# Kernel optimization log

Hardware: AMD Instinct MI355X
Metric: run time of the kernel (lower is better)

Reference implementation:

```python
import jax, jax.numpy as jnp
import numpy as np

B, N, C, H, W_, K, POS = 1, 100000, 128, 256, 256, 4, 36


def setup_inputs() -> dict:
    key = jax.random.key(0)
    ks = jax.random.split(key, 12)
    inp = {}
    # query coords in [-1, 1] (grid_sample normalized space)
    inp["query"] = jax.random.uniform(ks[0], (B, N, 3), jnp.float32, -1.0, 1.0)
    inp["pe"] = jax.random.normal(ks[1], (B, N, POS), jnp.float32)
    for i, p in enumerate(["xy", "xz", "yz"]):
        inp[f"feat_{p}"] = jax.random.normal(ks[2 + i], (B, C, H, W_), jnp.float32)
        inp[f"Wa_{p}"] = jax.random.normal(ks[5 + i], (POS, K), jnp.float32) * 0.1
        inp[f"ba_{p}"] = jnp.zeros((K,), jnp.float32)
        # offsets initialized to zero in the module; use small random so sampling is non-trivial
        inp[f"Wo_{p}"] = jax.random.normal(ks[8 + i], (POS, 2 * K), jnp.float32) * 0.02
        inp[f"bo_{p}"] = jnp.zeros((2 * K,), jnp.float32)
    return inp


def _bilinear_border(feat, gx, gy):
    """F.grid_sample(feat, grid, align_corners=False, padding_mode='border').
    feat: [B,C,H,W]; gx,gy: [B,N,K] normalized x (width) and y (height) coords.
    Returns [B,C,N,K]."""
    b, c, h, w = feat.shape
    # unnormalize (align_corners=False) then border-clip
    x = jnp.clip(((gx + 1.0) * w - 1.0) * 0.5, 0.0, w - 1.0)
    y = jnp.clip(((gy + 1.0) * h - 1.0) * 0.5, 0.0, h - 1.0)
    x0 = jnp.floor(x)
    y0 = jnp.floor(y)
    wx = x - x0  # [B,N,K]
    wy = y - y0
    xi0 = x0.astype(jnp.int32)
    yi0 = y0.astype(jnp.int32)
    xi1 = jnp.minimum(xi0 + 1, w - 1)
    yi1 = jnp.minimum(yi0 + 1, h - 1)
    ff = feat.reshape(b, c, h * w)
    gather = jax.vmap(lambda f, lin: f[:, lin])  # [C,HW],[N,K] -> [C,N,K]
    v00 = gather(ff, yi0 * w + xi0)
    v01 = gather(ff, yi0 * w + xi1)
    v10 = gather(ff, yi1 * w + xi0)
    v11 = gather(ff, yi1 * w + xi1)
    wx_ = wx[:, None]
    wy_ = wy[:, None]
    return (v00 * (1.0 - wx_) * (1.0 - wy_) + v01 * wx_ * (1.0 - wy_)
            + v10 * (1.0 - wx_) * wy_ + v11 * wx_ * wy_)


def _sample_plane(coords, pe, feat, Wa, ba, Wo, bo):
    b, n, _ = coords.shape
    attn = jax.nn.softmax(pe @ Wa + ba, axis=-1)            # [B,N,K]
    off = (pe @ Wo + bo).reshape(b, n, K, 2)                 # [B,N,K,2]
    sc = coords[:, :, None, :] + off                         # [B,N,K,2]
    # torch code flips last dim before grid_sample: grid x = sc[...,1], y = sc[...,0]
    sampled = _bilinear_border(feat, sc[..., 1], sc[..., 0])  # [B,C,N,K]
    out = jnp.einsum('bcnk,bnk->bnc', sampled, attn)         # weighted sum over K
    return out


def reference(query, pe, feat_xy, feat_xz, feat_yz,
              Wa_xy, ba_xy, Wo_xy, bo_xy,
              Wa_xz, ba_xz, Wo_xz, bo_xz,
              Wa_yz, ba_yz, Wo_yz, bo_yz):
    idx_xy = jnp.array([0, 1])
    idx_xz = jnp.array([0, 2])
    idx_yz = jnp.array([1, 2])
    f_xy = _sample_plane(query[..., idx_xy], pe, feat_xy, Wa_xy, ba_xy, Wo_xy, bo_xy)
    f_xz = _sample_plane(query[..., idx_xz], pe, feat_xz, Wa_xz, ba_xz, Wo_xz, bo_xz)
    f_yz = _sample_plane(query[..., idx_yz], pe, feat_yz, Wa_yz, ba_yz, Wo_yz, bo_yz)
    return f_xy + f_xz + f_yz
```

## Files before the change

kernel.cpp:

```cpp
#include <hip/hip_runtime.h>
#include <math.h>

#define NQ   100000
#define CCH  128
#define HDIM 256
#define WDIM 256
#define HW   (HDIM * WDIM)
#define KPTS 4
#define PDIM 36
#define NBIN 4096
#define RECW 40

__device__ inline unsigned int f2bf(float x) {
  unsigned int u = __float_as_uint(x);
  return (u + 0x7fffu + ((u >> 16) & 1u)) >> 16;
}

__device__ inline int axis_bin(float x) {
  int b = (int)((x + 1.0f) * 8.0f);
  return min(15, max(0, b));
}
__device__ inline unsigned int spread4(unsigned int x) {
  return (x & 1u) | ((x & 2u) << 2) | ((x & 4u) << 4) | ((x & 8u) << 6);
}
__device__ inline unsigned int bin_of(float x, float y, float z) {
  return spread4((unsigned int)axis_bin(x)) |
         (spread4((unsigned int)axis_bin(y)) << 1) |
         (spread4((unsigned int)axis_bin(z)) << 2);
}

__global__ void transpose_kernel(const float* __restrict__ f0,
                                 const float* __restrict__ f1,
                                 const float* __restrict__ f2,
                                 unsigned int* __restrict__ out) {
  __shared__ float tile[64][65];
  const int plane = blockIdx.z;
  const float* __restrict__ f = (plane == 0) ? f0 : ((plane == 1) ? f1 : f2);
  unsigned int* __restrict__ o = out + (size_t)plane * (size_t)HW * (CCH / 2);
  const int hw0 = blockIdx.x * 64;
  const int c0 = blockIdx.y * 64;
  const int t = threadIdx.x;
  const int c_l = t >> 6;
  const int hw_l = t & 63;
#pragma unroll
  for (int i = 0; i < 16; ++i) {
    tile[c_l + 4 * i][hw_l] = f[(size_t)(c0 + c_l + 4 * i) * HW + (hw0 + hw_l)];
  }
  __syncthreads();
#pragma unroll
  for (int i = 0; i < 8; ++i) {
    const int idx = t + 256 * i;
    const int j = idx & 31;
    const int r = idx >> 5;
    const unsigned int lo = f2bf(tile[2 * j][r]);
    const unsigned int hi = f2bf(tile[2 * j + 1][r]);
    o[(size_t)(hw0 + r) * (CCH / 2) + (c0 / 2 + j)] = (hi << 16) | lo;
  }
}

__global__ void zero_kernel(unsigned int* __restrict__ counts) {
  const int t = blockIdx.x * 256 + threadIdx.x;
  if (t < NBIN) counts[t] = 0;
}

__global__ void hist_kernel(const float* __restrict__ query,
                            unsigned int* __restrict__ counts) {
  const int q = blockIdx.x * 256 + threadIdx.x;
  if (q >= NQ) return;
  const unsigned int b = bin_of(query[q * 3 + 0], query[q * 3 + 1], query[q * 3 + 2]);
  atomicAdd(&counts[b], 1u);
}

__global__ void scan_kernel(const unsigned int* __restrict__ counts,
                            unsigned int* __restrict__ offs) {
  __shared__ unsigned int s[1024];
  const int t = threadIdx.x;
  const unsigned int c0 = counts[4 * t + 0];
  const unsigned int c1 = counts[4 * t + 1];
  const unsigned int c2 = counts[4 * t + 2];
  const unsigned int c3 = counts[4 * t + 3];
  const unsigned int sum = c0 + c1 + c2 + c3;
  s[t] = sum;
  __syncthreads();
  for (int d = 1; d < 1024; d <<= 1) {
    const unsigned int v = (t >= d) ? s[t - d] : 0u;
    __syncthreads();
    s[t] += v;
    __syncthreads();
  }
  const unsigned int base = s[t] - sum;
  offs[4 * t + 0] = base;
  offs[4 * t + 1] = base + c0;
  offs[4 * t + 2] = base + c0 + c1;
  offs[4 * t + 3] = base + c0 + c1 + c2;
}

__global__ void scatter_kernel(const float* __restrict__ query,
                               unsigned int* __restrict__ offs,
                               unsigned int* __restrict__ perm) {
  const int q = blockIdx.x * 256 + threadIdx.x;
  if (q >= NQ) return;
  const unsigned int b = bin_of(query[q * 3 + 0], query[q * 3 + 1], query[q * 3 + 2]);
  const unsigned int pos = atomicAdd(&offs[b], 1u);
  perm[pos] = (unsigned int)q;
}

__global__ void weights_kernel(const float* __restrict__ query,
                               const float* __restrict__ pe,
                               const unsigned int* __restrict__ perm,
                               const float* __restrict__ Wa0, const float* __restrict__ ba0,
                               const float* __restrict__ Wo0, const float* __restrict__ bo0,
                               const float* __restrict__ Wa1, const float* __restrict__ ba1,
                               const float* __restrict__ Wo1, const float* __restrict__ bo1,
                               const float* __restrict__ Wa2, const float* __restrict__ ba2,
                               const float* __restrict__ Wo2, const float* __restrict__ bo2,
                               float* __restrict__ rec) {
  __shared__ float sWa[3][PDIM][4];
  __shared__ float sWo[3][PDIM][8];
  __shared__ float sba[3][4];
  __shared__ float sbo[3][8];
  const int t = threadIdx.x;
  {
    float* wa = &sWa[0][0][0];
    for (int i = t; i < 144; i += 256) { wa[i] = Wa0[i]; wa[144 + i] = Wa1[i]; wa[288 + i] = Wa2[i]; }
    float* wo = &sWo[0][0][0];
    for (int i = t; i < 288; i += 256) { wo[i] = Wo0[i]; wo[288 + i] = Wo1[i]; wo[576 + i] = Wo2[i]; }
    if (t < 4) { sba[0][t] = ba0[t]; sba[1][t] = ba1[t]; sba[2][t] = ba2[t]; }
    if (t < 8) { sbo[0][t] = bo0[t]; sbo[1][t] = bo1[t]; sbo[2][t] = bo2[t]; }
  }
  __syncthreads();

  const int n = blockIdx.x * 256 + t;
  if (n >= NQ) return;
  const int q = (int)perm[n];

  float p[PDIM];
  const float4* pe4 = (const float4*)(pe + (size_t)q * PDIM);
#pragma unroll
  for (int i = 0; i < 9; ++i) {
    float4 v = pe4[i];
    p[4 * i + 0] = v.x; p[4 * i + 1] = v.y; p[4 * i + 2] = v.z; p[4 * i + 3] = v.w;
  }

  float la[3][4], of[3][8];
#pragma unroll
  for (int pl = 0; pl < 3; ++pl) {
#pragma unroll
    for (int k = 0; k < 4; ++k) la[pl][k] = sba[pl][k];
#pragma unroll
    for (int d = 0; d < 8; ++d) of[pl][d] = sbo[pl][d];
  }
#pragma unroll 4
  for (int j = 0; j < PDIM; ++j) {
    const float pj = p[j];
#pragma unroll
    for (int pl = 0; pl < 3; ++pl) {
#pragma unroll
      for (int k = 0; k < 4; ++k) la[pl][k] = fmaf(pj, sWa[pl][j][k], la[pl][k]);
#pragma unroll
      for (int d = 0; d < 8; ++d) of[pl][d] = fmaf(pj, sWo[pl][j][d], of[pl][d]);
    }
  }

  float* r = rec + (size_t)n * RECW;
  r[0] = query[q * 3 + 0];
  r[1] = query[q * 3 + 1];
  r[2] = query[q * 3 + 2];
  r[3] = __uint_as_float((unsigned int)q);
#pragma unroll
  for (int pl = 0; pl < 3; ++pl) {
    const float m = fmaxf(fmaxf(la[pl][0], la[pl][1]), fmaxf(la[pl][2], la[pl][3]));
    const float e0 = expf(la[pl][0] - m);
    const float e1 = expf(la[pl][1] - m);
    const float e2 = expf(la[pl][2] - m);
    const float e3 = expf(la[pl][3] - m);
    const float inv = 1.0f / (e0 + e1 + e2 + e3);
    r[4 + pl * 4 + 0] = e0 * inv;
    r[4 + pl * 4 + 1] = e1 * inv;
    r[4 + pl * 4 + 2] = e2 * inv;
    r[4 + pl * 4 + 3] = e3 * inv;
#pragma unroll
    for (int d = 0; d < 8; ++d) r[16 + pl * 8 + d] = of[pl][d];
  }
}

__global__ void sample_kernel(const float* __restrict__ rec,
                              const unsigned int* __restrict__ featT,
                              float* __restrict__ out) {
  const int lane = threadIdx.x & 63;
  const int wid = threadIdx.x >> 6;
  const int b = blockIdx.x;
  const int sb = (b & 7) * 3125 + (b >> 3);
  int i = sb * 4 + wid;
  i = __builtin_amdgcn_readfirstlane(i);
  if (i >= NQ) return;

  const float* __restrict__ r = rec + (size_t)i * RECW;
  const float qx = r[0];
  const float qy = r[1];
  const float qz = r[2];
  const int q = (int)__float_as_uint(r[3]);

  float at[12], of[24];
#pragma unroll
  for (int j = 0; j < 12; ++j) at[j] = r[4 + j];
#pragma unroll
  for (int j = 0; j < 24; ++j) of[j] = r[16 + j];

  float accx = 0.0f, accy = 0.0f;
#pragma unroll
  for (int pl = 0; pl < 3; ++pl) {
    const float ca = (pl == 2) ? qy : qx;
    const float cb = (pl == 0) ? qy : qz;
    const unsigned int* __restrict__ f =
        featT + (size_t)pl * (size_t)HW * (CCH / 2) + lane;
#pragma unroll
    for (int k = 0; k < KPTS; ++k) {
      const float gy = ca + of[pl * 8 + k * 2 + 0];
      const float gx = cb + of[pl * 8 + k * 2 + 1];
      float x = ((gx + 1.0f) * (float)WDIM - 1.0f) * 0.5f;
      float y = ((gy + 1.0f) * (float)HDIM - 1.0f) * 0.5f;
      x = fminf(fmaxf(x, 0.0f), (float)(WDIM - 1));
      y = fminf(fmaxf(y, 0.0f), (float)(HDIM - 1));
      const float x0f = floorf(x), y0f = floorf(y);
      const float wx = x - x0f, wy = y - y0f;
      const int xi0 = (int)x0f, yi0 = (int)y0f;
      const int xi1 = min(xi0 + 1, WDIM - 1);
      const int yi1 = min(yi0 + 1, HDIM - 1);
      const float a = at[pl * 4 + k];
      const float w00 = a * (1.0f - wx) * (1.0f - wy);
      const float w01 = a * wx * (1.0f - wy);
      const float w10 = a * (1.0f - wx) * wy;
      const float w11 = a * wx * wy;
      const int r0 = (yi0 * WDIM) * (CCH / 2);
      const int r1 = (yi1 * WDIM) * (CCH / 2);
      const unsigned int u00 = f[r0 + xi0 * (CCH / 2)];
      const unsigned int u01 = f[r0 + xi1 * (CCH / 2)];
      const unsigned int u10 = f[r1 + xi0 * (CCH / 2)];
      const unsigned int u11 = f[r1 + xi1 * (CCH / 2)];
      accx += w00 * __uint_as_float(u00 << 16) + w01 * __uint_as_float(u01 << 16) +
              w10 * __uint_as_float(u10 << 16) + w11 * __uint_as_float(u11 << 16);
      accy += w00 * __uint_as_float(u00 & 0xffff0000u) + w01 * __uint_as_float(u01 & 0xffff0000u) +
              w10 * __uint_as_float(u10 & 0xffff0000u) + w11 * __uint_as_float(u11 & 0xffff0000u);
    }
  }
  *(float2*)(out + (size_t)q * CCH + lane * 2) = make_float2(accx, accy);
}

__global__ void fused_fallback(const float* __restrict__ query,
                               const float* __restrict__ pe,
                               const float* __restrict__ f0,
                               const float* __restrict__ f1,
                               const float* __restrict__ f2,
                               const float* __restrict__ Wa0, const float* __restrict__ ba0,
                               const float* __restrict__ Wo0, const float* __restrict__ bo0,
                               const float* __restrict__ Wa1, const float* __restrict__ ba1,
                               const float* __restrict__ Wo1, const float* __restrict__ bo1,
                               const float* __restrict__ Wa2, const float* __restrict__ ba2,
                               const float* __restrict__ Wo2, const float* __restrict__ bo2,
                               float* __restrict__ out) {
  const int lane = threadIdx.x & 63;
  const int wid = threadIdx.x >> 6;
  int q = blockIdx.x * 4 + wid;
  q = __builtin_amdgcn_readfirstlane(q);
  if (q >= NQ) return;
  const float qx = query[q * 3 + 0];
  const float qy = query[q * 3 + 1];
  const float qz = query[q * 3 + 2];
  const float* pep = pe + (size_t)q * PDIM;
  const int c0i = lane * 2, c1i = lane * 2 + 1;
  float accx = 0.0f, accy = 0.0f;
#pragma unroll
  for (int pl = 0; pl < 3; ++pl) {
    const float* Wa = (pl == 0) ? Wa0 : ((pl == 1) ? Wa1 : Wa2);
    const float* ba = (pl == 0) ? ba0 : ((pl == 1) ? ba1 : ba2);
    const float* Wo = (pl == 0) ? Wo0 : ((pl == 1) ? Wo1 : Wo2);
    const float* bo = (pl == 0) ? bo0 : ((pl == 1) ? bo1 : bo2);
    const float* f = (pl == 0) ? f0 : ((pl == 1) ? f1 : f2);
    float la[4] = {ba[0], ba[1], ba[2], ba[3]};
    float of[8];
    for (int d = 0; d < 8; ++d) of[d] = bo[d];
    for (int j = 0; j < PDIM; ++j) {
      const float pj = pep[j];
      for (int k = 0; k < 4; ++k) la[k] = fmaf(pj, Wa[j * 4 + k], la[k]);
      for (int d = 0; d < 8; ++d) of[d] = fmaf(pj, Wo[j * 8 + d], of[d]);
    }
    const float m = fmaxf(fmaxf(la[0], la[1]), fmaxf(la[2], la[3]));
    float e[4], s = 0.0f;
    for (int k = 0; k < 4; ++k) { e[k] = expf(la[k] - m); s += e[k]; }
    const float inv = 1.0f / s;
    const float ca = (pl == 2) ? qy : qx;
    const float cb = (pl == 0) ? qy : qz;
    for (int k = 0; k < 4; ++k) {
      const float gy = ca + of[k * 2 + 0];
      const float gx = cb + of[k * 2 + 1];
      float x = ((gx + 1.0f) * (float)WDIM - 1.0f) * 0.5f;
      float y = ((gy + 1.0f) * (float)HDIM - 1.0f) * 0.5f;
      x = fminf(fmaxf(x, 0.0f), (float)(WDIM - 1));
      y = fminf(fmaxf(y, 0.0f), (float)(HDIM - 1));
      const float x0f = floorf(x), y0f = floorf(y);
      const float wx = x - x0f, wy = y - y0f;
      const int xi0 = (int)x0f, yi0 = (int)y0f;
      const int xi1 = min(xi0 + 1, WDIM - 1);
      const int yi1 = min(yi0 + 1, HDIM - 1);
      const float a = e[k] * inv;
      const float w00 = a * (1.0f - wx) * (1.0f - wy);
      const float w01 = a * wx * (1.0f - wy);
      const float w10 = a * (1.0f - wx) * wy;
      const float w11 = a * wx * wy;
      const size_t p00 = (size_t)(yi0 * WDIM + xi0);
      const size_t p01 = (size_t)(yi0 * WDIM + xi1);
      const size_t p10 = (size_t)(yi1 * WDIM + xi0);
      const size_t p11 = (size_t)(yi1 * WDIM + xi1);
      const float* fa = f + (size_t)c0i * HW;
      const float* fb = f + (size_t)c1i * HW;
      accx += w00 * fa[p00] + w01 * fa[p01] + w10 * fa[p10] + w11 * fa[p11];
      accy += w00 * fb[p00] + w01 * fb[p01] + w10 * fb[p10] + w11 * fb[p11];
    }
  }
  *(float2*)(out + (size_t)q * CCH + lane * 2) = make_float2(accx, accy);
}

extern "C" void kernel_launch(void* const* d_in, const int* in_sizes, int n_in,
                              void* d_out, int out_size, void* d_ws, size_t ws_size,
                              hipStream_t stream) {
  const float* query = (const float*)d_in[0];
  const float* pe    = (const float*)d_in[1];
  const float* feat0 = (const float*)d_in[2];
  const float* Wa0   = (const float*)d_in[3];
  const float* ba0   = (const float*)d_in[4];
  const float* Wo0   = (const float*)d_in[5];
  const float* bo0   = (const float*)d_in[6];
  const float* feat1 = (const float*)d_in[7];
  const float* Wa1   = (const float*)d_in[8];
  const float* ba1   = (const float*)d_in[9];
  const float* Wo1   = (const float*)d_in[10];
  const float* bo1   = (const float*)d_in[11];
  const float* feat2 = (const float*)d_in[12];
  const float* Wa2   = (const float*)d_in[13];
  const float* ba2   = (const float*)d_in[14];
  const float* Wo2   = (const float*)d_in[15];
  const float* bo2   = (const float*)d_in[16];
  float* out = (float*)d_out;

  const size_t featT_elems = 3ull * HW * (CCH / 2);
  const size_t need = featT_elems * 4 + (size_t)NQ * RECW * 4 +
                      (size_t)NBIN * 8 + (size_t)NQ * 4;

  if (ws_size >= need) {
    unsigned int* featT = (unsigned int*)d_ws;
    float* rec = (float*)(featT + featT_elems);
    unsigned int* counts = (unsigned int*)(rec + (size_t)NQ * RECW);
    unsigned int* offs = counts + NBIN;
    unsigned int* perm = offs + NBIN;

    zero_kernel<<<dim3((NBIN + 255) / 256), dim3(256), 0, stream>>>(counts);
    transpose_kernel<<<dim3(HW / 64, CCH / 64, 3), dim3(256), 0, stream>>>(
        feat0, feat1, feat2, featT);
    hist_kernel<<<dim3((NQ + 255) / 256), dim3(256), 0, stream>>>(query, counts);
    scan_kernel<<<dim3(1), dim3(1024), 0, stream>>>(counts, offs);
    scatter_kernel<<<dim3((NQ + 255) / 256), dim3(256), 0, stream>>>(query, offs, perm);
    weights_kernel<<<dim3((NQ + 255) / 256), dim3(256), 0, stream>>>(
        query, pe, perm, Wa0, ba0, Wo0, bo0, Wa1, ba1, Wo1, bo1,
        Wa2, ba2, Wo2, bo2, rec);
    sample_kernel<<<dim3(NQ / 4), dim3(256), 0, stream>>>(rec, featT, out);
  } else {
    fused_fallback<<<dim3((NQ + 3) / 4), dim3(256), 0, stream>>>(
        query, pe, feat0, feat1, feat2,
        Wa0, ba0, Wo0, bo0, Wa1, ba1, Wo1, bo1, Wa2, ba2, Wo2, bo2, out);
  }
}
```

Before: 155.2 us.

## Precompute bilinear weights and gather addresses in weights kernel; store features as fp16

Moves the bilinear coordinate math, attention-weighted corner weights and gather addresses into the per-query weights kernel, which writes them into a wider record. The sample kernel then only loads the precomputed weights and indices and does the gathers and FMAs. The transposed feature store switches from bf16 to fp16, which changes rounding and may overflow for large values. The wider record adds write and read traffic, and the sample kernel no longer checks the query index bound.

Result: no change. 157.8 us (+1.7%).

```diff
diff --git a/kernel.cpp b/kernel.cpp
--- a/kernel.cpp
+++ b/kernel.cpp
@@ -1,4 +1,5 @@
 #include <hip/hip_runtime.h>
+#include <hip/hip_fp16.h>
 #include <math.h>
 
 #define NQ   100000
@@ -9,12 +10,7 @@
 #define KPTS 4
 #define PDIM 36
 #define NBIN 4096
-#define RECW 40
-
-__device__ inline unsigned int f2bf(float x) {
-  unsigned int u = __float_as_uint(x);
-  return (u + 0x7fffu + ((u >> 16) & 1u)) >> 16;
-}
+#define RECW 100
 
 __device__ inline int axis_bin(float x) {
   int b = (int)((x + 1.0f) * 8.0f);
@@ -32,11 +28,11 @@
 __global__ void transpose_kernel(const float* __restrict__ f0,
                                  const float* __restrict__ f1,
                                  const float* __restrict__ f2,
-                                 unsigned int* __restrict__ out) {
+                                 __half2* __restrict__ out) {
   __shared__ float tile[64][65];
   const int plane = blockIdx.z;
   const float* __restrict__ f = (plane == 0) ? f0 : ((plane == 1) ? f1 : f2);
-  unsigned int* __restrict__ o = out + (size_t)plane * (size_t)HW * (CCH / 2);
+  __half2* __restrict__ o = out + (size_t)plane * (size_t)HW * (CCH / 2);
   const int hw0 = blockIdx.x * 64;
   const int c0 = blockIdx.y * 64;
   const int t = threadIdx.x;
@@ -52,9 +48,8 @@
     const int idx = t + 256 * i;
     const int j = idx & 31;
     const int r = idx >> 5;
-    const unsigned int lo = f2bf(tile[2 * j][r]);
-    const unsigned int hi = f2bf(tile[2 * j + 1][r]);
-    o[(size_t)(hw0 + r) * (CCH / 2) + (c0 / 2 + j)] = (hi << 16) | lo;
+    o[(size_t)(hw0 + r) * (CCH / 2) + (c0 / 2 + j)] =
+        __floats2half2_rn(tile[2 * j][r], tile[2 * j + 1][r]);
   }
 }
 
@@ -162,11 +157,14 @@
     }
   }
 
+  const float qx = query[q * 3 + 0];
+  const float qy = query[q * 3 + 1];
+  const float qz = query[q * 3 + 2];
+
   float* r = rec + (size_t)n * RECW;
-  r[0] = query[q * 3 + 0];
-  r[1] = query[q * 3 + 1];
-  r[2] = query[q * 3 + 2];
-  r[3] = __uint_as_float((unsigned int)q);
+  r[0] = __uint_as_float((unsigned int)q);
+  r[1] = 0.0f; r[2] = 0.0f; r[3] = 0.0f;
+
 #pragma unroll
   for (int pl = 0; pl < 3; ++pl) {
     const float m = fmaxf(fmaxf(la[pl][0], la[pl][1]), fmaxf(la[pl][2], la[pl][3]));
@@ -175,49 +173,15 @@
     const float e2 = expf(la[pl][2] - m);
     const float e3 = expf(la[pl][3] - m);
     const float inv = 1.0f / (e0 + e1 + e2 + e3);
-    r[4 + pl * 4 + 0] = e0 * inv;
-    r[4 + pl * 4 + 1] = e1 * inv;
-    r[4 + pl * 4 + 2] = e2 * inv;
-    r[4 + pl * 4 + 3] = e3 * inv;
-#pragma unroll
-    for (int d = 0; d < 8; ++d) r[16 + pl * 8 + d] = of[pl][d];
-  }
-}
-
-__global__ void sample_kernel(const float* __restrict__ rec,
-                              const unsigned int* __restrict__ featT,
-                              float* __restrict__ out) {
-  const int lane = threadIdx.x & 63;
-  const int wid = threadIdx.x >> 6;
-  const int b = blockIdx.x;
-  const int sb = (b & 7) * 3125 + (b >> 3);
-  int i = sb * 4 + wid;
-  i = __builtin_amdgcn_readfirstlane(i);
-  if (i >= NQ) return;
-
-  const float* __restrict__ r = rec + (size_t)i * RECW;
-  const float qx = r[0];
-  const float qy = r[1];
-  const float qz = r[2];
-  const int q = (int)__float_as_uint(r[3]);
-
-  float at[12], of[24];
-#pragma unroll
-  for (int j = 0; j < 12; ++j) at[j] = r[4 + j];
-#pragma unroll
-  for (int j = 0; j < 24; ++j) of[j] = r[16 + j];
-
-  float accx = 0.0f, accy = 0.0f;
-#pragma unroll
-  for (int pl = 0; pl < 3; ++pl) {
+    float at[4] = {e0 * inv, e1 * inv, e2 * inv, e3 * inv};
+
     const float ca = (pl == 2) ? qy : qx;
     const float cb = (pl == 0) ? qy : qz;
-    const unsigned int* __restrict__ f =
-        featT + (size_t)pl * (size_t)HW * (CCH / 2) + lane;
+    const unsigned int pbase = (unsigned int)pl * (unsigned int)HW * (CCH / 2);
 #pragma unroll
     for (int k = 0; k < KPTS; ++k) {
-      const float gy = ca + of[pl * 8 + k * 2 + 0];
-      const float gx = cb + of[pl * 8 + k * 2 + 1];
+      const float gy = ca + of[pl][k * 2 + 0];
+      const float gx = cb + of[pl][k * 2 + 1];
       float x = ((gx + 1.0f) * (float)WDIM - 1.0f) * 0.5f;
       float y = ((gy + 1.0f) * (float)HDIM - 1.0f) * 0.5f;
       x = fminf(fmaxf(x, 0.0f), (float)(WDIM - 1));
@@ -227,22 +191,57 @@
       const int xi0 = (int)x0f, yi0 = (int)y0f;
       const int xi1 = min(xi0 + 1, WDIM - 1);
       const int yi1 = min(yi0 + 1, HDIM - 1);
-      const float a = at[pl * 4 + k];
-      const float w00 = a * (1.0f - wx) * (1.0f - wy);
-      const float w01 = a * wx * (1.0f - wy);
-      const float w10 = a * (1.0f - wx) * wy;
-      const float w11 = a * wx * wy;
-      const int r0 = (yi0 * WDIM) * (CCH / 2);
-      const int r1 = (yi1 * WDIM) * (CCH / 2);
-      const unsigned int u00 = f[r0 + xi0 * (CCH / 2)];
-      const unsigned int u01 = f[r0 + xi1 * (CCH / 2)];
-      const unsigned int u10 = f[r1 + xi0 * (CCH / 2)];
-      const unsigned int u11 = f[r1 + xi1 * (CCH / 2)];
-      accx += w00 * __uint_as_float(u00 << 16) + w01 * __uint_as_float(u01 << 16) +
-              w10 * __uint_as_float(u10 << 16) + w11 * __uint_as_float(u11 << 16);
-      accy += w00 * __uint_as_float(u00 & 0xffff0000u) + w01 * __uint_as_float(u01 & 0xffff0000u) +
-              w10 * __uint_as_float(u10 & 0xffff0000u) + w11 * __uint_as_float(u11 & 0xffff0000u);
+      const float a = at[k];
+      float* g = r + 4 + 8 * (pl * 4 + k);
+      g[0] = a * (1.0f - wx) * (1.0f - wy);
+      g[1] = a * wx * (1.0f - wy);
+      g[2] = a * (1.0f - wx) * wy;
+      g[3] = a * wx * wy;
+      g[4] = __uint_as_float(pbase + (unsigned int)(yi0 * WDIM + xi0) * (CCH / 2));
+      g[5] = __uint_as_float(pbase + (unsigned int)(yi0 * WDIM + xi1) * (CCH / 2));
+      g[6] = __uint_as_float(pbase + (unsigned int)(yi1 * WDIM + xi0) * (CCH / 2));
+      g[7] = __uint_as_float(pbase + (unsigned int)(yi1 * WDIM + xi1) * (CCH / 2));
     }
+  }
+}
+
+__global__ void sample_kernel(const float* __restrict__ rec,
+                              const __half2* __restrict__ featT,
+                              float* __restrict__ out) {
+  const int lane = threadIdx.x & 63;
+  const int wid = threadIdx.x >> 6;
+  const int b = blockIdx.x;
+  const int sb = (b & 7) * 3125 + (b >> 3);
+  int i = sb * 4 + wid;
+  i = __builtin_amdgcn_readfirstlane(i);
+
+  const float* __restrict__ r = rec + (size_t)i * RECW;
+  const int q = (int)__float_as_uint(r[0]);
+  const __half2* __restrict__ fl = featT + lane;
+
+  float accx = 0.0f, accy = 0.0f;
+#pragma unroll
+  for (int j = 0; j < 12; ++j) {
+    const float w00 = r[4 + 8 * j + 0];
+    const float w01 = r[4 + 8 * j + 1];
+    const float w10 = r[4 + 8 * j + 2];
+    const float w11 = r[4 + 8 * j + 3];
+    const unsigned int a00 = __float_as_uint(r[4 + 8 * j + 4]);
+    const unsigned int a01 = __float_as_uint(r[4 + 8 * j + 5]);
+    const unsigned int a10 = __float_as_uint(r[4 + 8 * j + 6]);
+    const unsigned int a11 = __float_as_uint(r[4 + 8 * j + 7]);
+    const __half2 v00 = fl[a00];
+    const __half2 v01 = fl[a01];
+    const __half2 v10 = fl[a10];
+    const __half2 v11 = fl[a11];
+    accx = fmaf(w00, __low2float(v00), accx);
+    accy = fmaf(w00, __high2float(v00), accy);
+    accx = fmaf(w01, __low2float(v01), accx);
+    accy = fmaf(w01, __high2float(v01), accy);
+    accx = fmaf(w10, __low2float(v10), accx);
+    accy = fmaf(w10, __high2float(v10), accy);
+    accx = fmaf(w11, __low2float(v11), accx);
+    accy = fmaf(w11, __high2float(v11), accy);
   }
   *(float2*)(out + (size_t)q * CCH + lane * 2) = make_float2(accx, accy);
 }
@@ -348,7 +347,7 @@
                       (size_t)NBIN * 8 + (size_t)NQ * 4;
 
   if (ws_size >= need) {
-    unsigned int* featT = (unsigned int*)d_ws;
+    __half2* featT = (__half2*)d_ws;
     float* rec = (float*)(featT + featT_elems);
     unsigned int* counts = (unsigned int*)(rec + (size_t)NQ * RECW);
     unsigned int* offs = counts + NBIN;
```
